# Kernel tuning notes

Hardware: AMD Instinct MI355X
Metric: run time of the kernel (lower is better)

## Reference

```python
import jax, jax.numpy as jnp
import numpy as np

BATCH, L, ED, N = 2, 2048, 1024, 16

def setup_inputs() -> dict:
    key = jax.random.key(0)
    ks = jax.random.split(key, 6)
    x = jax.random.normal(ks[0], (BATCH, L, ED), dtype=jnp.float32)
    # delta > 0 (as after softplus in Mamba); small to keep exp products stable
    delta = jax.random.uniform(ks[1], (BATCH, L, ED), dtype=jnp.float32) * 0.1
    # A < 0 so deltaA = exp(delta*A) in (0,1): stable decaying recurrence
    A = -jax.random.uniform(ks[2], (ED, N), dtype=jnp.float32) - 0.5
    B = jax.random.normal(ks[3], (BATCH, L, N), dtype=jnp.float32)
    C = jax.random.normal(ks[4], (BATCH, L, N), dtype=jnp.float32)
    D = jax.random.normal(ks[5], (ED,), dtype=jnp.float32)
    return {"x": x, "delta": delta, "A": A, "B": B, "C": C, "D": D}

def reference(x, delta, A, B, C, D):
    # x, delta: (b, l, ed); A: (ed, n); B, C: (b, l, n); D: (ed,)
    deltaA = jnp.exp(delta[..., None] * A)                    # (b, l, ed, n)
    BX = (delta[..., None] * B[:, :, None, :]) * x[..., None]  # (b, l, ed, n)

    # linear recurrence h_t = deltaA_t * h_{t-1} + BX_t via associative scan
    def combine(c1, c2):
        a1, b1 = c1
        a2, b2 = c2
        return a2 * a1, a2 * b1 + b2

    _, hs = jax.lax.associative_scan(combine, (deltaA, BX), axis=1)  # (b, l, ed, n)
    y = jnp.einsum("blen,bln->ble", hs, C) + D * x             # (b, l, ed)
    return y
```

## Files before the change

kernel.cpp:

```cpp
#include <hip/hip_runtime.h>


#define LOG2E 1.4426950408889634f

#if __has_builtin(__builtin_amdgcn_exp2f)
#define EXP2F(xx) __builtin_amdgcn_exp2f(xx)
#else
#define EXP2F(xx) exp2f(xx)
#endif

constexpr int BATCH = 2;
constexpr int SEQ   = 2048;
constexpr int ED    = 1024;
constexpr int NS    = 16;

constexpr int NC  = 64;
constexpr int CT  = SEQ / NC;
constexpr int EDG = 256;
constexpr int NEG = ED / EDG;

__global__ __launch_bounds__(EDG, 2) void ssm_pass1(
    const float* __restrict__ x, const float* __restrict__ dl,
    const float* __restrict__ A, const float* __restrict__ B,
    float* __restrict__ Q, float* __restrict__ Dsum)
{
    const int c = blockIdx.x, g = blockIdx.y, b = blockIdx.z;
    const int tid = threadIdx.x;
    const int ed = g * EDG + tid;

    __shared__ alignas(16) float Bs[CT * NS];
    const long tbase = (long)b * SEQ + (long)c * CT;
    for (int i = tid; i < CT * NS; i += EDG) Bs[i] = B[tbase * NS + i];
    __syncthreads();

    float A2[NS];
    {
        const float4* Ap = reinterpret_cast<const float4*>(A + (long)ed * NS);
        #pragma unroll
        for (int k = 0; k < 4; ++k) {
            float4 a4 = Ap[k];
            A2[4*k+0] = a4.x * LOG2E; A2[4*k+1] = a4.y * LOG2E;
            A2[4*k+2] = a4.z * LOG2E; A2[4*k+3] = a4.w * LOG2E;
        }
    }

    float h[NS];
    #pragma unroll
    for (int n = 0; n < NS; ++n) h[n] = 0.f;
    float dsum = 0.f;

    const float* dp = dl + tbase * ED + ed;
    const float* xp = x  + tbase * ED + ed;

    float da[4], xa[4];
    #pragma unroll
    for (int j = 0; j < 4; ++j) { da[j] = dp[(long)j * ED]; xa[j] = xp[(long)j * ED]; }

    for (int tg = 0; tg < CT / 4; ++tg) {
        float dn[4], xn[4];
        if (tg < CT / 4 - 1) {
            #pragma unroll
            for (int j = 0; j < 4; ++j) {
                dn[j] = dp[(long)((tg + 1) * 4 + j) * ED];
                xn[j] = xp[(long)((tg + 1) * 4 + j) * ED];
            }
        }
        #pragma unroll
        for (int j = 0; j < 4; ++j) {
            const int t = tg * 4 + j;
            float dlt = da[j], xv = xa[j];
            dsum += dlt;
            float dx = dlt * xv;
            const float4* Bs4 = reinterpret_cast<const float4*>(&Bs[t * NS]);
            #pragma unroll
            for (int k = 0; k < 4; ++k) {
                float4 b4 = Bs4[k];
                h[4*k+0] = fmaf(EXP2F(dlt * A2[4*k+0]), h[4*k+0], dx * b4.x);
                h[4*k+1] = fmaf(EXP2F(dlt * A2[4*k+1]), h[4*k+1], dx * b4.y);
                h[4*k+2] = fmaf(EXP2F(dlt * A2[4*k+2]), h[4*k+2], dx * b4.z);
                h[4*k+3] = fmaf(EXP2F(dlt * A2[4*k+3]), h[4*k+3], dx * b4.w);
            }
        }
        #pragma unroll
        for (int j = 0; j < 4; ++j) { da[j] = dn[j]; xa[j] = xn[j]; }
    }

    const long qo = ((long)(c * BATCH + b) * ED + ed) * NS;
    float4* Qp = reinterpret_cast<float4*>(Q + qo);
    #pragma unroll
    for (int k = 0; k < 4; ++k)
        Qp[k] = make_float4(h[4*k+0], h[4*k+1], h[4*k+2], h[4*k+3]);
    Dsum[(long)(c * BATCH + b) * ED + ed] = dsum;
}

__global__ __launch_bounds__(128) void ssm_pass2(
    const float* __restrict__ A, const float* __restrict__ Q,
    const float* __restrict__ Dsum, float* __restrict__ Hprev)
{
    const int idx = blockIdx.x * 128 + threadIdx.x;
    const int n  = idx & (NS - 1);
    const int ed = (idx >> 4) & (ED - 1);
    const int b  = idx >> 14;

    const float a2 = A[(long)ed * NS + n] * LOG2E;
    const long strideQ = (long)BATCH * ED * NS;
    const long strideD = (long)BATCH * ED;
    const long o0 = ((long)b * ED + ed) * NS + n;
    const long d0 = (long)b * ED + ed;

    float h = 0.f;
    float qs[8], ds[8];
    #pragma unroll
    for (int j = 0; j < 8; ++j) {
        qs[j] = Q[o0 + (long)j * strideQ];
        ds[j] = Dsum[d0 + (long)j * strideD];
    }
    for (int gi = 0; gi < NC / 8; ++gi) {
        float qn[8], dn[8];
        if (gi < NC / 8 - 1) {
            #pragma unroll
            for (int j = 0; j < 8; ++j) {
                qn[j] = Q[o0 + (long)((gi + 1) * 8 + j) * strideQ];
                dn[j] = Dsum[d0 + (long)((gi + 1) * 8 + j) * strideD];
            }
        }
        float ps[8];
        #pragma unroll
        for (int j = 0; j < 8; ++j) ps[j] = EXP2F(a2 * ds[j]);
        #pragma unroll
        for (int j = 0; j < 8; ++j) {
            Hprev[o0 + (long)(gi * 8 + j) * strideQ] = h;
            h = fmaf(ps[j], h, qs[j]);
        }
        #pragma unroll
        for (int j = 0; j < 8; ++j) { qs[j] = qn[j]; ds[j] = dn[j]; }
    }
}

__global__ __launch_bounds__(EDG, 2) void ssm_pass3(
    const float* __restrict__ x, const float* __restrict__ dl,
    const float* __restrict__ A, const float* __restrict__ B,
    const float* __restrict__ C, const float* __restrict__ Dv,
    const float* __restrict__ Hprev, float* __restrict__ y)
{
    const int c = blockIdx.x, g = blockIdx.y, b = blockIdx.z;
    const int tid = threadIdx.x;
    const int ed = g * EDG + tid;

    __shared__ alignas(16) float Bs[CT * NS];
    __shared__ alignas(16) float Cs[CT * NS];
    const long tbase = (long)b * SEQ + (long)c * CT;
    for (int i = tid; i < CT * NS; i += EDG) {
        Bs[i] = B[tbase * NS + i];
        Cs[i] = C[tbase * NS + i];
    }
    __syncthreads();

    float A2[NS];
    {
        const float4* Ap = reinterpret_cast<const float4*>(A + (long)ed * NS);
        #pragma unroll
        for (int k = 0; k < 4; ++k) {
            float4 a4 = Ap[k];
            A2[4*k+0] = a4.x * LOG2E; A2[4*k+1] = a4.y * LOG2E;
            A2[4*k+2] = a4.z * LOG2E; A2[4*k+3] = a4.w * LOG2E;
        }
    }

    float h[NS];
    {
        const long qo = ((long)(c * BATCH + b) * ED + ed) * NS;
        const float4* Hp = reinterpret_cast<const float4*>(Hprev + qo);
        #pragma unroll
        for (int k = 0; k < 4; ++k) {
            float4 h4 = Hp[k];
            h[4*k+0] = h4.x; h[4*k+1] = h4.y; h[4*k+2] = h4.z; h[4*k+3] = h4.w;
        }
    }
    const float dvec = Dv[ed];

    const float* dp = dl + tbase * ED + ed;
    const float* xp = x  + tbase * ED + ed;
    float* yp = y + tbase * ED + ed;

    float da[4], xa[4];
    #pragma unroll
    for (int j = 0; j < 4; ++j) { da[j] = dp[(long)j * ED]; xa[j] = xp[(long)j * ED]; }

    for (int tg = 0; tg < CT / 4; ++tg) {
        float dn[4], xn[4];
        if (tg < CT / 4 - 1) {
            #pragma unroll
            for (int j = 0; j < 4; ++j) {
                dn[j] = dp[(long)((tg + 1) * 4 + j) * ED];
                xn[j] = xp[(long)((tg + 1) * 4 + j) * ED];
            }
        }
        #pragma unroll
        for (int j = 0; j < 4; ++j) {
            const int t = tg * 4 + j;
            float dlt = da[j], xv = xa[j];
            float dx = dlt * xv;
            float acc = dvec * xv;
            const float4* Bs4 = reinterpret_cast<const float4*>(&Bs[t * NS]);
            const float4* Cs4 = reinterpret_cast<const float4*>(&Cs[t * NS]);
            #pragma unroll
            for (int k = 0; k < 4; ++k) {
                float4 b4 = Bs4[k];
                float4 c4 = Cs4[k];
                h[4*k+0] = fmaf(EXP2F(dlt * A2[4*k+0]), h[4*k+0], dx * b4.x);
                acc = fmaf(h[4*k+0], c4.x, acc);
                h[4*k+1] = fmaf(EXP2F(dlt * A2[4*k+1]), h[4*k+1], dx * b4.y);
                acc = fmaf(h[4*k+1], c4.y, acc);
                h[4*k+2] = fmaf(EXP2F(dlt * A2[4*k+2]), h[4*k+2], dx * b4.z);
                acc = fmaf(h[4*k+2], c4.z, acc);
                h[4*k+3] = fmaf(EXP2F(dlt * A2[4*k+3]), h[4*k+3], dx * b4.w);
                acc = fmaf(h[4*k+3], c4.w, acc);
            }
            yp[(long)t * ED] = acc;
        }
        #pragma unroll
        for (int j = 0; j < 4; ++j) { da[j] = dn[j]; xa[j] = xn[j]; }
    }
}

__global__ __launch_bounds__(EDG) void ssm_fallback(
    const float* __restrict__ x, const float* __restrict__ dl,
    const float* __restrict__ A, const float* __restrict__ B,
    const float* __restrict__ C, const float* __restrict__ Dv,
    float* __restrict__ y)
{
    const int g = blockIdx.x, b = blockIdx.y;
    const int ed = g * EDG + threadIdx.x;

    float A2[NS];
    {
        const float4* Ap = reinterpret_cast<const float4*>(A + (long)ed * NS);
        #pragma unroll
        for (int k = 0; k < 4; ++k) {
            float4 a4 = Ap[k];
            A2[4*k+0] = a4.x * LOG2E; A2[4*k+1] = a4.y * LOG2E;
            A2[4*k+2] = a4.z * LOG2E; A2[4*k+3] = a4.w * LOG2E;
        }
    }
    float h[NS];
    #pragma unroll
    for (int n = 0; n < NS; ++n) h[n] = 0.f;
    const float dvec = Dv[ed];

    for (int t = 0; t < SEQ; ++t) {
        const long tb = (long)b * SEQ + t;
        float dlt = dl[tb * ED + ed];
        float xv  = x[tb * ED + ed];
        float dx = dlt * xv;
        float acc = dvec * xv;
        const float4* Bp = reinterpret_cast<const float4*>(B + tb * NS);
        const float4* Cp = reinterpret_cast<const float4*>(C + tb * NS);
        #pragma unroll
        for (int k = 0; k < 4; ++k) {
            float4 b4 = Bp[k];
            float4 c4 = Cp[k];
            h[4*k+0] = fmaf(EXP2F(dlt * A2[4*k+0]), h[4*k+0], dx * b4.x);
            acc = fmaf(h[4*k+0], c4.x, acc);
            h[4*k+1] = fmaf(EXP2F(dlt * A2[4*k+1]), h[4*k+1], dx * b4.y);
            acc = fmaf(h[4*k+1], c4.y, acc);
            h[4*k+2] = fmaf(EXP2F(dlt * A2[4*k+2]), h[4*k+2], dx * b4.z);
            acc = fmaf(h[4*k+2], c4.z, acc);
            h[4*k+3] = fmaf(EXP2F(dlt * A2[4*k+3]), h[4*k+3], dx * b4.w);
            acc = fmaf(h[4*k+3], c4.w, acc);
        }
        y[tb * ED + ed] = acc;
    }
}

extern "C" void kernel_launch(void* const* d_in, const int* in_sizes, int n_in,
                              void* d_out, int out_size, void* d_ws, size_t ws_size,
                              hipStream_t stream) {
    const float* x  = (const float*)d_in[0];
    const float* dl = (const float*)d_in[1];
    const float* A  = (const float*)d_in[2];
    const float* B  = (const float*)d_in[3];
    const float* C  = (const float*)d_in[4];
    const float* Dv = (const float*)d_in[5];
    float* y = (float*)d_out;

    const size_t qElems = (size_t)NC * BATCH * ED * NS;
    const size_t dElems = (size_t)NC * BATCH * ED;
    const size_t need = (2 * qElems + dElems) * sizeof(float);

    if (ws_size >= need) {
        float* Q     = (float*)d_ws;
        float* Hprev = Q + qElems;
        float* Dsum  = Hprev + qElems;
        ssm_pass1<<<dim3(NC, NEG, BATCH), EDG, 0, stream>>>(x, dl, A, B, Q, Dsum);
        ssm_pass2<<<(BATCH * ED * NS) / 128, 128, 0, stream>>>(A, Q, Dsum, Hprev);
        ssm_pass3<<<dim3(NC, NEG, BATCH), EDG, 0, stream>>>(x, dl, A, B, C, Dv, Hprev, y);
    } else {
        ssm_fallback<<<dim3(NEG, BATCH), EDG, 0, stream>>>(x, dl, A, B, C, Dv, y);
    }
}
```

Baseline: 114.3 us.

## Process two channels per thread and double chunk count in chunked scan

Each thread in pass1 and pass3 now handles two adjacent channels, using float2 loads and stores for delta, x and y and reusing each shared-memory B/C read across both channels. The chunk count is doubled, which halves the per-chunk sequential length and keeps the grid size roughly the same. This aims to raise memory-access width and instruction-level parallelism, since two independent recurrences can interleave. In exchange, pass2 has a longer serial carry across chunks, the Q/Hprev intermediates are larger, and register pressure per thread roughly doubles.

```diff
diff --git a/kernel.cpp b/kernel.cpp
--- a/kernel.cpp
+++ b/kernel.cpp
@@ -14,10 +14,12 @@
 constexpr int ED    = 1024;
 constexpr int NS    = 16;
 
-constexpr int NC  = 64;
+constexpr int NC  = 128;
 constexpr int CT  = SEQ / NC;
 constexpr int EDG = 256;
-constexpr int NEG = ED / EDG;
+constexpr int EPT = 2;
+constexpr int EDB = EDG * EPT;
+constexpr int NEG = ED / EDB;
 
 __global__ __launch_bounds__(EDG, 2) void ssm_pass1(
     const float* __restrict__ x, const float* __restrict__ dl,
@@ -26,71 +28,83 @@
 {
     const int c = blockIdx.x, g = blockIdx.y, b = blockIdx.z;
     const int tid = threadIdx.x;
-    const int ed = g * EDG + tid;
+    const int ed0 = g * EDB + tid * EPT;
 
     __shared__ alignas(16) float Bs[CT * NS];
     const long tbase = (long)b * SEQ + (long)c * CT;
     for (int i = tid; i < CT * NS; i += EDG) Bs[i] = B[tbase * NS + i];
     __syncthreads();
 
-    float A2[NS];
+    float A2x[NS], A2y[NS];
     {
-        const float4* Ap = reinterpret_cast<const float4*>(A + (long)ed * NS);
-        #pragma unroll
-        for (int k = 0; k < 4; ++k) {
-            float4 a4 = Ap[k];
-            A2[4*k+0] = a4.x * LOG2E; A2[4*k+1] = a4.y * LOG2E;
-            A2[4*k+2] = a4.z * LOG2E; A2[4*k+3] = a4.w * LOG2E;
-        }
-    }
-
-    float h[NS];
-    #pragma unroll
-    for (int n = 0; n < NS; ++n) h[n] = 0.f;
-    float dsum = 0.f;
-
-    const float* dp = dl + tbase * ED + ed;
-    const float* xp = x  + tbase * ED + ed;
-
-    float da[4], xa[4];
-    #pragma unroll
-    for (int j = 0; j < 4; ++j) { da[j] = dp[(long)j * ED]; xa[j] = xp[(long)j * ED]; }
+        const float4* Ax = reinterpret_cast<const float4*>(A + (long)ed0 * NS);
+        const float4* Ay = reinterpret_cast<const float4*>(A + (long)(ed0 + 1) * NS);
+        #pragma unroll
+        for (int k = 0; k < 4; ++k) {
+            float4 ax = Ax[k], ay = Ay[k];
+            A2x[4*k+0] = ax.x * LOG2E; A2x[4*k+1] = ax.y * LOG2E;
+            A2x[4*k+2] = ax.z * LOG2E; A2x[4*k+3] = ax.w * LOG2E;
+            A2y[4*k+0] = ay.x * LOG2E; A2y[4*k+1] = ay.y * LOG2E;
+            A2y[4*k+2] = ay.z * LOG2E; A2y[4*k+3] = ay.w * LOG2E;
+        }
+    }
+
+    float hx[NS], hy[NS];
+    #pragma unroll
+    for (int n = 0; n < NS; ++n) { hx[n] = 0.f; hy[n] = 0.f; }
+    float dsx = 0.f, dsy = 0.f;
+
+    const float2* dp = reinterpret_cast<const float2*>(dl + tbase * ED + ed0);
+    const float2* xp = reinterpret_cast<const float2*>(x  + tbase * ED + ed0);
+    constexpr int RS = ED / 2;
+
+    float2 da[4], xa[4];
+    #pragma unroll
+    for (int j = 0; j < 4; ++j) { da[j] = dp[(long)j * RS]; xa[j] = xp[(long)j * RS]; }
 
     for (int tg = 0; tg < CT / 4; ++tg) {
-        float dn[4], xn[4];
+        float2 dn[4], xn[4];
         if (tg < CT / 4 - 1) {
             #pragma unroll
             for (int j = 0; j < 4; ++j) {
-                dn[j] = dp[(long)((tg + 1) * 4 + j) * ED];
-                xn[j] = xp[(long)((tg + 1) * 4 + j) * ED];
+                dn[j] = dp[(long)((tg + 1) * 4 + j) * RS];
+                xn[j] = xp[(long)((tg + 1) * 4 + j) * RS];
             }
         }
         #pragma unroll
         for (int j = 0; j < 4; ++j) {
             const int t = tg * 4 + j;
-            float dlt = da[j], xv = xa[j];
-            dsum += dlt;
-            float dx = dlt * xv;
+            const float2 d2 = da[j], x2 = xa[j];
+            dsx += d2.x; dsy += d2.y;
+            const float dxx = d2.x * x2.x, dxy = d2.y * x2.y;
             const float4* Bs4 = reinterpret_cast<const float4*>(&Bs[t * NS]);
             #pragma unroll
             for (int k = 0; k < 4; ++k) {
                 float4 b4 = Bs4[k];
-                h[4*k+0] = fmaf(EXP2F(dlt * A2[4*k+0]), h[4*k+0], dx * b4.x);
-                h[4*k+1] = fmaf(EXP2F(dlt * A2[4*k+1]), h[4*k+1], dx * b4.y);
-                h[4*k+2] = fmaf(EXP2F(dlt * A2[4*k+2]), h[4*k+2], dx * b4.z);
-                h[4*k+3] = fmaf(EXP2F(dlt * A2[4*k+3]), h[4*k+3], dx * b4.w);
+                hx[4*k+0] = fmaf(EXP2F(d2.x * A2x[4*k+0]), hx[4*k+0], dxx * b4.x);
+                hy[4*k+0] = fmaf(EXP2F(d2.y * A2y[4*k+0]), hy[4*k+0], dxy * b4.x);
+                hx[4*k+1] = fmaf(EXP2F(d2.x * A2x[4*k+1]), hx[4*k+1], dxx * b4.y);
+                hy[4*k+1] = fmaf(EXP2F(d2.y * A2y[4*k+1]), hy[4*k+1], dxy * b4.y);
+                hx[4*k+2] = fmaf(EXP2F(d2.x * A2x[4*k+2]), hx[4*k+2], dxx * b4.z);
+                hy[4*k+2] = fmaf(EXP2F(d2.y * A2y[4*k+2]), hy[4*k+2], dxy * b4.z);
+                hx[4*k+3] = fmaf(EXP2F(d2.x * A2x[4*k+3]), hx[4*k+3], dxx * b4.w);
+                hy[4*k+3] = fmaf(EXP2F(d2.y * A2y[4*k+3]), hy[4*k+3], dxy * b4.w);
             }
         }
         #pragma unroll
         for (int j = 0; j < 4; ++j) { da[j] = dn[j]; xa[j] = xn[j]; }
     }
 
-    const long qo = ((long)(c * BATCH + b) * ED + ed) * NS;
-    float4* Qp = reinterpret_cast<float4*>(Q + qo);
-    #pragma unroll
-    for (int k = 0; k < 4; ++k)
-        Qp[k] = make_float4(h[4*k+0], h[4*k+1], h[4*k+2], h[4*k+3]);
-    Dsum[(long)(c * BATCH + b) * ED + ed] = dsum;
+    const long qbase = ((long)(c * BATCH + b) * ED + ed0) * NS;
+    float4* Qx = reinterpret_cast<float4*>(Q + qbase);
+    float4* Qy = reinterpret_cast<float4*>(Q + qbase + NS);
+    #pragma unroll
+    for (int k = 0; k < 4; ++k) {
+        Qx[k] = make_float4(hx[4*k+0], hx[4*k+1], hx[4*k+2], hx[4*k+3]);
+        Qy[k] = make_float4(hy[4*k+0], hy[4*k+1], hy[4*k+2], hy[4*k+3]);
+    }
+    float2* Dp = reinterpret_cast<float2*>(Dsum + (long)(c * BATCH + b) * ED + ed0);
+    *Dp = make_float2(dsx, dsy);
 }
 
 __global__ __launch_bounds__(128) void ssm_pass2(
@@ -145,7 +159,7 @@
 {
     const int c = blockIdx.x, g = blockIdx.y, b = blockIdx.z;
     const int tid = threadIdx.x;
-    const int ed = g * EDG + tid;
+    const int ed0 = g * EDB + tid * EPT;
 
     __shared__ alignas(16) float Bs[CT * NS];
     __shared__ alignas(16) float Cs[CT * NS];
@@ -156,68 +170,82 @@
     }
     __syncthreads();
 
-    float A2[NS];
+    float A2x[NS], A2y[NS];
     {
-        const float4* Ap = reinterpret_cast<const float4*>(A + (long)ed * NS);
-        #pragma unroll
-        for (int k = 0; k < 4; ++k) {
-            float4 a4 = Ap[k];
-            A2[4*k+0] = a4.x * LOG2E; A2[4*k+1] = a4.y * LOG2E;
-            A2[4*k+2] = a4.z * LOG2E; A2[4*k+3] = a4.w * LOG2E;
-        }
-    }
-
-    float h[NS];
+        const float4* Ax = reinterpret_cast<const float4*>(A + (long)ed0 * NS);
+        const float4* Ay = reinterpret_cast<const float4*>(A + (long)(ed0 + 1) * NS);
+        #pragma unroll
+        for (int k = 0; k < 4; ++k) {
+            float4 ax = Ax[k], ay = Ay[k];
+            A2x[4*k+0] = ax.x * LOG2E; A2x[4*k+1] = ax.y * LOG2E;
+            A2x[4*k+2] = ax.z * LOG2E; A2x[4*k+3] = ax.w * LOG2E;
+            A2y[4*k+0] = ay.x * LOG2E; A2y[4*k+1] = ay.y * LOG2E;
+            A2y[4*k+2] = ay.z * LOG2E; A2y[4*k+3] = ay.w * LOG2E;
+        }
+    }
+
+    float hx[NS], hy[NS];
     {
-        const long qo = ((long)(c * BATCH + b) * ED + ed) * NS;
-        const float4* Hp = reinterpret_cast<const float4*>(Hprev + qo);
-        #pragma unroll
-        for (int k = 0; k < 4; ++k) {
-            float4 h4 = Hp[k];
-            h[4*k+0] = h4.x; h[4*k+1] = h4.y; h[4*k+2] = h4.z; h[4*k+3] = h4.w;
-        }
-    }
-    const float dvec = Dv[ed];
-
-    const float* dp = dl + tbase * ED + ed;
-    const float* xp = x  + tbase * ED + ed;
-    float* yp = y + tbase * ED + ed;
-
-    float da[4], xa[4];
-    #pragma unroll
-    for (int j = 0; j < 4; ++j) { da[j] = dp[(long)j * ED]; xa[j] = xp[(long)j * ED]; }
+        const long qbase = ((long)(c * BATCH + b) * ED + ed0) * NS;
+        const float4* Hx = reinterpret_cast<const float4*>(Hprev + qbase);
+        const float4* Hy = reinterpret_cast<const float4*>(Hprev + qbase + NS);
+        #pragma unroll
+        for (int k = 0; k < 4; ++k) {
+            float4 h4x = Hx[k], h4y = Hy[k];
+            hx[4*k+0] = h4x.x; hx[4*k+1] = h4x.y; hx[4*k+2] = h4x.z; hx[4*k+3] = h4x.w;
+            hy[4*k+0] = h4y.x; hy[4*k+1] = h4y.y; hy[4*k+2] = h4y.z; hy[4*k+3] = h4y.w;
+        }
+    }
+    const float2 dvec = *reinterpret_cast<const float2*>(Dv + ed0);
+
+    const float2* dp = reinterpret_cast<const float2*>(dl + tbase * ED + ed0);
+    const float2* xp = reinterpret_cast<const float2*>(x  + tbase * ED + ed0);
+    float2* yp = reinterpret_cast<float2*>(y + tbase * ED + ed0);
+    constexpr int RS = ED / 2;
+
+    float2 da[4], xa[4];
+    #pragma unroll
+    for (int j = 0; j < 4; ++j) { da[j] = dp[(long)j * RS]; xa[j] = xp[(long)j * RS]; }
 
     for (int tg = 0; tg < CT / 4; ++tg) {
-        float dn[4], xn[4];
+        float2 dn[4], xn[4];
         if (tg < CT / 4 - 1) {
             #pragma unroll
             for (int j = 0; j < 4; ++j) {
-                dn[j] = dp[(long)((tg + 1) * 4 + j) * ED];
-                xn[j] = xp[(long)((tg + 1) * 4 + j) * ED];
+                dn[j] = dp[(long)((tg + 1) * 4 + j) * RS];
+                xn[j] = xp[(long)((tg + 1) * 4 + j) * RS];
             }
         }
         #pragma unroll
         for (int j = 0; j < 4; ++j) {
             const int t = tg * 4 + j;
-            float dlt = da[j], xv = xa[j];
-            float dx = dlt * xv;
-            float acc = dvec * xv;
+            const float2 d2 = da[j], x2 = xa[j];
+            const float dxx = d2.x * x2.x, dxy = d2.y * x2.y;
+            float accx = dvec.x * x2.x, accy = dvec.y * x2.y;
             const float4* Bs4 = reinterpret_cast<const float4*>(&Bs[t * NS]);
             const float4* Cs4 = reinterpret_cast<const float4*>(&Cs[t * NS]);
             #pragma unroll
             for (int k = 0; k < 4; ++k) {
                 float4 b4 = Bs4[k];
                 float4 c4 = Cs4[k];
-                h[4*k+0] = fmaf(EXP2F(dlt * A2[4*k+0]), h[4*k+0], dx * b4.x);
-                acc = fmaf(h[4*k+0], c4.x, acc);
-                h[4*k+1] = fmaf(EXP2F(dlt * A2[4*k+1]), h[4*k+1], dx * b4.y);
-                acc = fmaf(h[4*k+1], c4.y, acc);
-                h[4*k+2] = fmaf(EXP2F(dlt * A2[4*k+2]), h[4*k+2], dx * b4.z);
-                acc = fmaf(h[4*k+2], c4.z, acc);
-                h[4*k+3] = fmaf(EXP2F(dlt * A2[4*k+3]), h[4*k+3], dx * b4.w);
-                acc = fmaf(h[4*k+3], c4.w, acc);
-            }
-            yp[(long)t * ED] = acc;
+                hx[4*k+0] = fmaf(EXP2F(d2.x * A2x[4*k+0]), hx[4*k+0], dxx * b4.x);
+                hy[4*k+0] = fmaf(EXP2F(d2.y * A2y[4*k+0]), hy[4*k+0], dxy * b4.x);
+                accx = fmaf(hx[4*k+0], c4.x, accx);
+                accy = fmaf(hy[4*k+0], c4.x, accy);
+                hx[4*k+1] = fmaf(EXP2F(d2.x * A2x[4*k+1]), hx[4*k+1], dxx * b4.y);
+                hy[4*k+1] = fmaf(EXP2F(d2.y * A2y[4*k+1]), hy[4*k+1], dxy * b4.y);
+                accx = fmaf(hx[4*k+1], c4.y, accx);
+                accy = fmaf(hy[4*k+1], c4.y, accy);
+                hx[4*k+2] = fmaf(EXP2F(d2.x * A2x[4*k+2]), hx[4*k+2], dxx * b4.z);
+                hy[4*k+2] = fmaf(EXP2F(d2.y * A2y[4*k+2]), hy[4*k+2], dxy * b4.z);
+                accx = fmaf(hx[4*k+2], c4.z, accx);
+                accy = fmaf(hy[4*k+2], c4.z, accy);
+                hx[4*k+3] = fmaf(EXP2F(d2.x * A2x[4*k+3]), hx[4*k+3], dxx * b4.w);
+                hy[4*k+3] = fmaf(EXP2F(d2.y * A2y[4*k+3]), hy[4*k+3], dxy * b4.w);
+                accx = fmaf(hx[4*k+3], c4.w, accx);
+                accy = fmaf(hy[4*k+3], c4.w, accy);
+            }
+            yp[(long)t * RS] = make_float2(accx, accy);
         }
         #pragma unroll
         for (int j = 0; j < 4; ++j) { da[j] = dn[j]; xa[j] = xn[j]; }
```

Measured after the change: 136.0 us. 1.19x slower.
